# Optimization experiments

Measured on AMD Instinct MI355X. Metric: run time of the kernel, lower is better.

Reference implementation:

```python
import jax, jax.numpy as jnp
import numpy as np

N, F_IN, E = 50000, 256, 1000000
UNITS, HEADS, LAYERS, OUT = 32, 8, 2, 64
D = UNITS * HEADS  # 256


def setup_inputs() -> dict:
    key = jax.random.key(0)
    ks = jax.random.split(key, 12)
    node_states = jax.random.normal(ks[0], (1, N, F_IN), dtype=jnp.float32)
    # edges sorted by source column (required by the tf.repeat/bincount trick)
    src = jnp.sort(jax.random.randint(ks[1], (E,), 0, N, dtype=jnp.int32))
    dst = jax.random.randint(ks[2], (E,), 0, N, dtype=jnp.int32)
    edges = jnp.stack([src, dst], axis=-1)[None]  # [1, E, 2]
    edge_weights = jax.random.uniform(ks[3], (1, E), dtype=jnp.float32)
    pos_cls = jax.random.randint(ks[4], (1, 128), 0, N, dtype=jnp.int32)
    s = 0.05
    Wp = jax.random.normal(ks[5], (F_IN, D), dtype=jnp.float32) * s
    bp = jnp.zeros((D,), dtype=jnp.float32)
    Wk = jax.random.normal(ks[6], (LAYERS, HEADS, D, UNITS), dtype=jnp.float32) * s
    Wa = jax.random.normal(ks[7], (LAYERS, HEADS, 2 * UNITS, 1), dtype=jnp.float32) * s
    Wo = jax.random.normal(ks[8], (D, OUT), dtype=jnp.float32) * s
    bo = jnp.zeros((OUT,), dtype=jnp.float32)
    return {
        "node_states": node_states, "edges": edges, "edge_weights": edge_weights,
        "pos_cls": pos_cls, "Wp": Wp, "bp": bp, "Wk": Wk, "Wa": Wa,
        "Wo": Wo, "bo": bo,
    }


def _gat_head(x, src, dst, ew, W, a, n_nodes):
    xt = x @ W  # [N, U]
    # edge features: concat(src_feat, dst_feat) scaled by edge weight
    ef = jnp.concatenate([xt[src], xt[dst]], axis=-1) * ew[:, None]  # [E, 2U]
    s = jax.nn.leaky_relu((ef @ a)[:, 0], negative_slope=0.2)        # [E]
    s = jnp.exp(jnp.clip(s, -2.0, 2.0))
    ssum = jax.ops.segment_sum(s, src, num_segments=n_nodes)          # [N]
    norm = s / ssum[src]
    return jax.ops.segment_sum(xt[dst] * norm[:, None], src, num_segments=n_nodes)


def reference(node_states, edges, edge_weights, pos_cls, Wp, bp, Wk, Wa, Wo, bo):
    x0 = node_states[0]        # [N, F_in]
    e = edges[0]               # [E, 2]
    ew = edge_weights[0]       # [E]
    src, dst = e[:, 0], e[:, 1]
    n_nodes = x0.shape[0]
    x = jax.nn.relu(x0 @ Wp + bp)  # [N, D]
    n_layers, n_heads = Wk.shape[0], Wk.shape[1]
    for l in range(n_layers):
        heads = [_gat_head(x, src, dst, ew, Wk[l, h], Wa[l, h], n_nodes)
                 for h in range(n_heads)]
        mh = jax.nn.relu(jnp.concatenate(heads, axis=-1))  # [N, D]
        x = mh + x  # residual
    out = x @ Wo + bo
    return out[None]  # [1, N, OUT]
```

## Files before the change

kernel.cpp:

```cpp
#include <hip/hip_runtime.h>
#include <hip/hip_bf16.h>
#include <math.h>

#define N_NODES 50000
#define F_DIM 256
#define NE 1000000
#define N_HEADS 8
#define M_PAD 50048

typedef __attribute__((ext_vector_type(8))) short short8;
typedef __attribute__((ext_vector_type(4))) float floatx4;
typedef __attribute__((ext_vector_type(2))) float floatx2;

__device__ __forceinline__ void load16_lds(const void* g, void* l) {
    __builtin_amdgcn_global_load_lds(
        (const __attribute__((address_space(1))) unsigned int*)(unsigned long long)g,
        (__attribute__((address_space(3))) unsigned int*)(unsigned int)(unsigned long long)l,
        16, 0, 0);
}

__device__ __forceinline__ unsigned int pack2bf(float a, float b) {
    __hip_bfloat16 t0 = __float2bfloat16(a), t1 = __float2bfloat16(b);
    unsigned short u0, u1;
    __builtin_memcpy(&u0, &t0, 2);
    __builtin_memcpy(&u1, &t1, 2);
    return (unsigned int)u0 | ((unsigned int)u1 << 16);
}

__device__ __forceinline__ float bf_lo(unsigned int u) {
    return __uint_as_float(u << 16);
}
__device__ __forceinline__ float bf_hi(unsigned int u) {
    return __uint_as_float(u & 0xffff0000u);
}

__device__ __forceinline__ unsigned int pack4fp8(float x, float y, float z,
                                                 float w) {
    int v = __builtin_amdgcn_cvt_pk_fp8_f32(x, y, 0, false);
    v = __builtin_amdgcn_cvt_pk_fp8_f32(z, w, v, true);
    return (unsigned int)v;
}

__global__ __launch_bounds__(256) void prep_kernel(
    const float* __restrict__ node_states, const int* __restrict__ edges,
    const float* __restrict__ ew, const float* __restrict__ Wp,
    const float* __restrict__ Wk, const float* __restrict__ Wo,
    __hip_bfloat16* __restrict__ xt16, int2* __restrict__ edata,
    __hip_bfloat16* __restrict__ wpT, __hip_bfloat16* __restrict__ wkT,
    __hip_bfloat16* __restrict__ woT, int* __restrict__ row_start) {
    const int b = blockIdx.x;
    const int tid = threadIdx.x;
    if (b < 12500) {
        const size_t i = ((size_t)b * 256 + tid) * 4;
        const float4 v = *(const float4*)(node_states + i);
        uint2 pk;
        pk.x = pack2bf(v.x, v.y);
        pk.y = pack2bf(v.z, v.w);
        *(uint2*)((unsigned short*)xt16 + i) = pk;
    } else if (b < 16407) {
        const int e = (b - 12500) * 256 + tid;
        if (e < NE) {
            int2 d;
            d.x = edges[2 * e + 1];
            d.y = __float_as_int(ew[e]);
            edata[e] = d;
        }
    } else if (b < 17239) {
        const int wb = b - 16407;
        if (wb < 256) {
            int idx = wb * 256 + tid;
            int n = idx >> 8, k = idx & 255;
            wpT[idx] = __float2bfloat16(Wp[k * 256 + n]);
        } else if (wb < 768) {
            int idx = (wb - 256) * 256 + tid;
            int l = idx >> 16, n = (idx >> 8) & 255, k = idx & 255;
            int h = n >> 5, u = n & 31;
            wkT[idx] = __float2bfloat16(Wk[(((l * 8 + h) * 256) + k) * 32 + u]);
        } else {
            int idx = (wb - 768) * 256 + tid;
            int n = idx >> 8, k = idx & 255;
            woT[idx] = __float2bfloat16(Wo[k * 64 + n]);
        }
    } else {
        const int i = (b - 17239) * 256 + tid;
        if (i > N_NODES) return;
        if (i == N_NODES) { row_start[N_NODES] = NE; return; }
        int lo = 0, hi = NE;
        while (lo < hi) {
            int mid = (lo + hi) >> 1;
            if (edges[2 * mid] < i) lo = mid + 1; else hi = mid;
        }
        row_start[i] = lo;
    }
}

template <bool BIAS_RELU, bool FP8OUT, bool ALPHA>
__global__ __launch_bounds__(256) void gemm_mfma(
    const __hip_bfloat16* __restrict__ A16, const __hip_bfloat16* __restrict__ BT,
    const float* __restrict__ bias, void* __restrict__ Y,
    const float* __restrict__ Wa_l, float* __restrict__ a_srcO,
    float* __restrict__ a_dstO) {
    __shared__ __align__(16) short lA[128 * 32];
    __shared__ __align__(16) short lB[128 * 32];
    const int tid = threadIdx.x;
    const int row0 = blockIdx.x * 128;
    const int n0 = blockIdx.y * 128;
    const int w = tid >> 6, l = tid & 63;
    const int wr = w >> 1, wc = w & 1;

    const __hip_bfloat16* gA = A16 + (size_t)(row0 + (tid >> 2)) * 256 + (tid & 3) * 8;
    const __hip_bfloat16* gB = BT + (size_t)(n0 + (tid >> 2)) * 256 + (tid & 3) * 8;
    short* dA = lA + tid * 8;
    short* dB = lB + tid * 8;

    floatx4 acc[4][4] = {};

    const short* pa = lA + (wr * 64 + (l & 15)) * 32 + (l >> 4) * 8;
    const short* pb = lB + (wc * 64 + (l & 15)) * 32 + (l >> 4) * 8;

    for (int kk = 0; kk < 8; ++kk) {
        const int ko = kk * 32;
        load16_lds(gA + ko, dA);
        load16_lds(gA + 64 * 256 + ko, dA + 256 * 8);
        load16_lds(gB + ko, dB);
        load16_lds(gB + 64 * 256 + ko, dB + 256 * 8);
        __syncthreads();
        short8 af[4], bf[4];
#pragma unroll
        for (int t = 0; t < 4; ++t) {
            af[t] = *(const short8*)(pa + t * 16 * 32);
            bf[t] = *(const short8*)(pb + t * 16 * 32);
        }
#pragma unroll
        for (int mt = 0; mt < 4; ++mt)
#pragma unroll
            for (int nt = 0; nt < 4; ++nt)
                acc[mt][nt] = __builtin_amdgcn_mfma_f32_16x16x32_bf16(
                    bf[nt], af[mt], acc[mt][nt], 0, 0, 0);
        __syncthreads();
    }

    const int m_base = row0 + wr * 64 + (l & 15);
    const int n_base = n0 + wc * 64 + ((l >> 4) << 2);
#pragma unroll
    for (int mt = 0; mt < 4; ++mt) {
        const int m = m_base + mt * 16;
        if (m >= N_NODES) continue;
#pragma unroll
        for (int nt = 0; nt < 4; ++nt) {
            const int n = n_base + nt * 16;
            floatx4 v = acc[mt][nt];
            if (BIAS_RELU) {
                const float4 bb = *(const float4*)(bias + n);
                v.x = fmaxf(v.x + bb.x, 0.f);
                v.y = fmaxf(v.y + bb.y, 0.f);
                v.z = fmaxf(v.z + bb.z, 0.f);
                v.w = fmaxf(v.w + bb.w, 0.f);
            }
            if constexpr (FP8OUT) {
                *((unsigned int*)Y + ((((size_t)m << 8) + n) >> 2)) =
                    pack4fp8(v.x, v.y, v.z, v.w);
            } else {
                uint2 pk;
                pk.x = pack2bf(v.x, v.y);
                pk.y = pack2bf(v.z, v.w);
                *(uint2*)((unsigned short*)Y + ((size_t)m << 8) + n) = pk;
            }
        }
    }

    if constexpr (ALPHA) {
        const int lg = l >> 4;
        float4 wS[2][2], wD[2][2];
#pragma unroll
        for (int hl = 0; hl < 2; ++hl) {
            const int h = (n0 >> 5) + wc * 2 + hl;
#pragma unroll
            for (int p = 0; p < 2; ++p) {
                wS[hl][p] = *(const float4*)(Wa_l + h * 64 + p * 16 + lg * 4);
                wD[hl][p] =
                    *(const float4*)(Wa_l + h * 64 + 32 + p * 16 + lg * 4);
            }
        }
        float aS[4][2], aD[4][2];
#pragma unroll
        for (int mt = 0; mt < 4; ++mt)
#pragma unroll
            for (int hl = 0; hl < 2; ++hl) {
                float s = 0.f, d = 0.f;
#pragma unroll
                for (int p = 0; p < 2; ++p) {
                    const floatx4 v = acc[mt][2 * hl + p];
                    const float4 ws = wS[hl][p], wd = wD[hl][p];
                    s += v.x * ws.x + v.y * ws.y + v.z * ws.z + v.w * ws.w;
                    d += v.x * wd.x + v.y * wd.y + v.z * wd.z + v.w * wd.w;
                }
                s += __shfl_xor(s, 16);
                s += __shfl_xor(s, 32);
                d += __shfl_xor(d, 16);
                d += __shfl_xor(d, 32);
                aS[mt][hl] = s;
                aD[mt][hl] = d;
            }
        if (lg == 0) {
#pragma unroll
            for (int mt = 0; mt < 4; ++mt) {
                const int m = m_base + mt * 16;
#pragma unroll
                for (int hl = 0; hl < 2; ++hl) {
                    const int h = (n0 >> 5) + wc * 2 + hl;
                    a_srcO[(size_t)m * 8 + h] = aS[mt][hl];
                    a_dstO[(size_t)m * 8 + h] = aD[mt][hl];
                }
            }
        }
    }
}

__global__ __launch_bounds__(256) void gemm_mfma_out(
    const __hip_bfloat16* __restrict__ A16, const __hip_bfloat16* __restrict__ BT,
    const float* __restrict__ bias, float* __restrict__ out) {
    __shared__ __align__(16) short lA[128 * 32];
    __shared__ __align__(16) short lB[64 * 32];
    const int tid = threadIdx.x;
    const int row0 = blockIdx.x * 128;
    const int w = tid >> 6, l = tid & 63;

    const __hip_bfloat16* gA = A16 + (size_t)(row0 + (tid >> 2)) * 256 + (tid & 3) * 8;
    const __hip_bfloat16* gB = BT + (size_t)(tid >> 2) * 256 + (tid & 3) * 8;
    short* dA = lA + tid * 8;
    short* dB = lB + tid * 8;

    floatx4 acc[2][4] = {};

    const short* pa = lA + (w * 32 + (l & 15)) * 32 + (l >> 4) * 8;
    const short* pb = lB + (l & 15) * 32 + (l >> 4) * 8;

    for (int kk = 0; kk < 8; ++kk) {
        const int ko = kk * 32;
        load16_lds(gA + ko, dA);
        load16_lds(gA + 64 * 256 + ko, dA + 256 * 8);
        load16_lds(gB + ko, dB);
        __syncthreads();
        short8 af[2], bf[4];
#pragma unroll
        for (int t = 0; t < 2; ++t) af[t] = *(const short8*)(pa + t * 16 * 32);
#pragma unroll
        for (int t = 0; t < 4; ++t) bf[t] = *(const short8*)(pb + t * 16 * 32);
#pragma unroll
        for (int mt = 0; mt < 2; ++mt)
#pragma unroll
            for (int nt = 0; nt < 4; ++nt)
                acc[mt][nt] = __builtin_amdgcn_mfma_f32_16x16x32_bf16(
                    bf[nt], af[mt], acc[mt][nt], 0, 0, 0);
        __syncthreads();
    }

    const int m_base = row0 + w * 32 + (l & 15);
    const int n_base = (l >> 4) << 2;
#pragma unroll
    for (int mt = 0; mt < 2; ++mt) {
        const int m = m_base + mt * 16;
        if (m >= N_NODES) continue;
#pragma unroll
        for (int nt = 0; nt < 4; ++nt) {
            const int n = n_base + nt * 16;
            const float4 bb = *(const float4*)(bias + n);
            floatx4 v = acc[mt][nt];
            float4 o = {v.x + bb.x, v.y + bb.y, v.z + bb.z, v.w + bb.w};
            *(float4*)(&out[(size_t)m * 64 + n]) = o;
        }
    }
}

__device__ __forceinline__ float edge_score(float asrc, float ad, float w) {
    float sp = (asrc + ad) * w;
    sp = (sp >= 0.f) ? sp : 0.2f * sp;
    sp = fminf(fmaxf(sp, -2.f), 2.f);
    return __expf(sp);
}

#define ACC8(u, s)                                               \
    {                                                            \
        const floatx2 f01 = __builtin_amdgcn_cvt_pk_f32_fp8(u, false); \
        const floatx2 f23 = __builtin_amdgcn_cvt_pk_f32_fp8(u, true);  \
        a0 = fmaf(f01.x, s, a0);                                 \
        a1 = fmaf(f01.y, s, a1);                                 \
        a2 = fmaf(f23.x, s, a2);                                 \
        a3 = fmaf(f23.y, s, a3);                                 \
    }

__global__ __launch_bounds__(256) void edge_kernel(
    const unsigned long long* __restrict__ edata,
    const int* __restrict__ row_start, const unsigned int* __restrict__ xt8,
    const float* __restrict__ a_src, const float* __restrict__ a_dst,
    __hip_bfloat16* __restrict__ xb16) {
    const int tid = threadIdx.x;
    const int node =
        __builtin_amdgcn_readfirstlane(blockIdx.x * 4 + (tid >> 6));
    const int l = tid & 63;
    const int h = l >> 3;
    const float asrc = a_src[node * N_HEADS + h];
    const int e0 = row_start[node], e1 = row_start[node + 1];

    unsigned long long* xrow =
        (unsigned long long*)((unsigned short*)xb16 + (size_t)node * 256 +
                              l * 4);
    const unsigned long long xin = __builtin_nontemporal_load(xrow);

    float a0 = 0.f, a1 = 0.f, a2 = 0.f, a3 = 0.f, ssum = 0.f;
    int e = e0;
    for (; e + 4 <= e1; e += 4) {
        const unsigned long long ed0 = __builtin_nontemporal_load(edata + e);
        const unsigned long long ed1 = __builtin_nontemporal_load(edata + e + 1);
        const unsigned long long ed2 = __builtin_nontemporal_load(edata + e + 2);
        const unsigned long long ed3 = __builtin_nontemporal_load(edata + e + 3);
        const int d0 = (int)(unsigned int)ed0;
        const int d1 = (int)(unsigned int)ed1;
        const int d2 = (int)(unsigned int)ed2;
        const int d3 = (int)(unsigned int)ed3;
        const float w0 = __uint_as_float((unsigned int)(ed0 >> 32));
        const float w1 = __uint_as_float((unsigned int)(ed1 >> 32));
        const float w2 = __uint_as_float((unsigned int)(ed2 >> 32));
        const float w3 = __uint_as_float((unsigned int)(ed3 >> 32));
        const float s0 = edge_score(asrc, a_dst[d0 * N_HEADS + h], w0);
        const float s1 = edge_score(asrc, a_dst[d1 * N_HEADS + h], w1);
        const float s2 = edge_score(asrc, a_dst[d2 * N_HEADS + h], w2);
        const float s3 = edge_score(asrc, a_dst[d3 * N_HEADS + h], w3);
        const unsigned int u0 = xt8[(size_t)d0 * 64 + l];
        const unsigned int u1 = xt8[(size_t)d1 * 64 + l];
        const unsigned int u2 = xt8[(size_t)d2 * 64 + l];
        const unsigned int u3 = xt8[(size_t)d3 * 64 + l];
        ACC8(u0, s0);
        ACC8(u1, s1);
        ACC8(u2, s2);
        ACC8(u3, s3);
        ssum += (s0 + s1) + (s2 + s3);
    }
    for (; e < e1; ++e) {
        const unsigned long long ed = __builtin_nontemporal_load(edata + e);
        const int d = (int)(unsigned int)ed;
        const float w = __uint_as_float((unsigned int)(ed >> 32));
        const float s = edge_score(asrc, a_dst[d * N_HEADS + h], w);
        const unsigned int u = xt8[(size_t)d * 64 + l];
        ACC8(u, s);
        ssum += s;
    }
    const float inv = (e1 > e0) ? 1.f / ssum : 0.f;
    const unsigned int xlo = (unsigned int)xin;
    const unsigned int xhi = (unsigned int)(xin >> 32);
    const float c0 = bf_lo(xlo) + fmaxf(a0 * inv, 0.f);
    const float c1 = bf_hi(xlo) + fmaxf(a1 * inv, 0.f);
    const float c2 = bf_lo(xhi) + fmaxf(a2 * inv, 0.f);
    const float c3 = bf_hi(xhi) + fmaxf(a3 * inv, 0.f);
    const unsigned long long pk =
        (unsigned long long)pack2bf(c0, c1) |
        ((unsigned long long)pack2bf(c2, c3) << 32);
    __builtin_nontemporal_store(pk, xrow);
}

extern "C" void kernel_launch(void* const* d_in, const int* in_sizes, int n_in,
                              void* d_out, int out_size, void* d_ws,
                              size_t ws_size, hipStream_t stream) {
    const float* node_states = (const float*)d_in[0];
    const int* edges = (const int*)d_in[1];
    const float* ew = (const float*)d_in[2];
    const float* Wp = (const float*)d_in[4];
    const float* bp = (const float*)d_in[5];
    const float* Wk = (const float*)d_in[6];
    const float* Wa = (const float*)d_in[7];
    const float* Wo = (const float*)d_in[8];
    const float* bo = (const float*)d_in[9];
    float* out = (float*)d_out;

    char* ws = (char*)d_ws;
    __hip_bfloat16* xb16 = (__hip_bfloat16*)ws; ws += (size_t)M_PAD * 256 * 2;
    __hip_bfloat16* xt16 = (__hip_bfloat16*)ws; ws += (size_t)M_PAD * 256 * 2;
    unsigned int* xt8 = (unsigned int*)ws;      ws += (size_t)M_PAD * 256;
    int2* edata = (int2*)ws;                    ws += (size_t)NE * 8;
    float* a_src = (float*)ws;                  ws += (size_t)M_PAD * N_HEADS * 4;
    float* a_dst = (float*)ws;                  ws += (size_t)M_PAD * N_HEADS * 4;
    __hip_bfloat16* wpT = (__hip_bfloat16*)ws;  ws += 65536 * 2;
    __hip_bfloat16* wkT = (__hip_bfloat16*)ws;  ws += 131072 * 2;
    __hip_bfloat16* woT = (__hip_bfloat16*)ws;  ws += 16384 * 2;
    int* row_st = (int*)ws;

    prep_kernel<<<17435, 256, 0, stream>>>(node_states, edges, ew, Wp, Wk, Wo,
                                           xt16, edata, wpT, wkT, woT, row_st);

    gemm_mfma<true, false, false><<<dim3((N_NODES + 127) / 128, 2), 256, 0,
                                    stream>>>(xt16, wpT, bp, xb16, nullptr,
                                              nullptr, nullptr);

    gemm_mfma<false, true, true><<<dim3((N_NODES + 127) / 128, 2), 256, 0,
                                   stream>>>(xb16, wkT, nullptr, xt8, Wa,
                                             a_src, a_dst);
    edge_kernel<<<N_NODES / 4, 256, 0, stream>>>(
        (const unsigned long long*)edata, row_st, xt8, a_src, a_dst, xb16);

    gemm_mfma<false, true, true><<<dim3((N_NODES + 127) / 128, 2), 256, 0,
                                   stream>>>(xb16, wkT + 65536, nullptr, xt8,
                                             Wa + 512, a_src, a_dst);
    edge_kernel<<<N_NODES / 4, 256, 0, stream>>>(
        (const unsigned long long*)edata, row_st, xt8, a_src, a_dst, xb16);

    gemm_mfma_out<<<(N_NODES + 127) / 128, 256, 0, stream>>>(xb16, woT, bo, out);
}
```

Before: 298.1 us.

## Compute edge scores cooperatively across lanes and broadcast via bpermute in edge kernel

Each wavefront previously had every lane compute the score of every edge for its own head, which is 8x redundant work per head group. Now the 64 lanes are split into 8 edge slots by 8 heads, so each lane computes one (edge, head) score per batch of 8 edges. Scores are broadcast with ds_bpermute and destination ids with readlane, and the softmax denominator is reduced with xor shuffles. This cuts the redundant a_dst gathers and exp work, at the cost of cross-lane permutes and readlanes on every edge.

Result: no change. 303.7 us (+1.9%).

```diff
diff --git a/kernel.cpp b/kernel.cpp
--- a/kernel.cpp
+++ b/kernel.cpp
@@ -299,53 +299,64 @@
     const int node =
         __builtin_amdgcn_readfirstlane(blockIdx.x * 4 + (tid >> 6));
     const int l = tid & 63;
-    const int h = l >> 3;
-    const float asrc = a_src[node * N_HEADS + h];
-    const int e0 = row_start[node], e1 = row_start[node + 1];
+    const int hf = l >> 3;
+    const int hs = l & 7;
+    const int slot = l >> 3;
+    const int e0 = __builtin_amdgcn_readfirstlane(row_start[node]);
+    const int e1 = __builtin_amdgcn_readfirstlane(row_start[node + 1]);
+    const float asrc = a_src[(size_t)node * 8 + hs];
+    const int baddr = hf << 2;
 
     unsigned long long* xrow =
         (unsigned long long*)((unsigned short*)xb16 + (size_t)node * 256 +
                               l * 4);
     const unsigned long long xin = __builtin_nontemporal_load(xrow);
 
-    float a0 = 0.f, a1 = 0.f, a2 = 0.f, a3 = 0.f, ssum = 0.f;
-    int e = e0;
-    for (; e + 4 <= e1; e += 4) {
-        const unsigned long long ed0 = __builtin_nontemporal_load(edata + e);
-        const unsigned long long ed1 = __builtin_nontemporal_load(edata + e + 1);
-        const unsigned long long ed2 = __builtin_nontemporal_load(edata + e + 2);
-        const unsigned long long ed3 = __builtin_nontemporal_load(edata + e + 3);
-        const int d0 = (int)(unsigned int)ed0;
-        const int d1 = (int)(unsigned int)ed1;
-        const int d2 = (int)(unsigned int)ed2;
-        const int d3 = (int)(unsigned int)ed3;
-        const float w0 = __uint_as_float((unsigned int)(ed0 >> 32));
-        const float w1 = __uint_as_float((unsigned int)(ed1 >> 32));
-        const float w2 = __uint_as_float((unsigned int)(ed2 >> 32));
-        const float w3 = __uint_as_float((unsigned int)(ed3 >> 32));
-        const float s0 = edge_score(asrc, a_dst[d0 * N_HEADS + h], w0);
-        const float s1 = edge_score(asrc, a_dst[d1 * N_HEADS + h], w1);
-        const float s2 = edge_score(asrc, a_dst[d2 * N_HEADS + h], w2);
-        const float s3 = edge_score(asrc, a_dst[d3 * N_HEADS + h], w3);
-        const unsigned int u0 = xt8[(size_t)d0 * 64 + l];
-        const unsigned int u1 = xt8[(size_t)d1 * 64 + l];
-        const unsigned int u2 = xt8[(size_t)d2 * 64 + l];
-        const unsigned int u3 = xt8[(size_t)d3 * 64 + l];
-        ACC8(u0, s0);
-        ACC8(u1, s1);
-        ACC8(u2, s2);
-        ACC8(u3, s3);
-        ssum += (s0 + s1) + (s2 + s3);
-    }
-    for (; e < e1; ++e) {
-        const unsigned long long ed = __builtin_nontemporal_load(edata + e);
-        const int d = (int)(unsigned int)ed;
+    float a0 = 0.f, a1 = 0.f, a2 = 0.f, a3 = 0.f, ssp = 0.f;
+    int eb = e0;
+    for (; eb + 8 <= e1; eb += 8) {
+        const unsigned long long ed =
+            __builtin_nontemporal_load(edata + eb + slot);
+        const int dd = (int)(unsigned int)ed;
         const float w = __uint_as_float((unsigned int)(ed >> 32));
-        const float s = edge_score(asrc, a_dst[d * N_HEADS + h], w);
-        const unsigned int u = xt8[(size_t)d * 64 + l];
-        ACC8(u, s);
-        ssum += s;
-    }
+        const float s = edge_score(asrc, a_dst[(size_t)dd * 8 + hs], w);
+        ssp += s;
+        const int sbits = (int)__float_as_uint(s);
+#pragma unroll
+        for (int j = 0; j < 8; ++j) {
+            const float sj = __uint_as_float(
+                (unsigned int)__builtin_amdgcn_ds_bpermute(baddr + (j << 5),
+                                                           sbits));
+            const int dj = __builtin_amdgcn_readlane(dd, j * 8);
+            const unsigned int u = xt8[(size_t)dj * 64 + l];
+            ACC8(u, sj);
+        }
+    }
+    if (eb < e1) {
+        const int ecl = min(eb + slot, e1 - 1);
+        const unsigned long long ed = __builtin_nontemporal_load(edata + ecl);
+        const int dd = (int)(unsigned int)ed;
+        const float w = __uint_as_float((unsigned int)(ed >> 32));
+        float s = edge_score(asrc, a_dst[(size_t)dd * 8 + hs], w);
+        s = (eb + slot < e1) ? s : 0.f;
+        ssp += s;
+        const int sbits = (int)__float_as_uint(s);
+        const int jmax = e1 - eb;
+        for (int j = 0; j < jmax; ++j) {
+            const float sj = __uint_as_float(
+                (unsigned int)__builtin_amdgcn_ds_bpermute(baddr + (j << 5),
+                                                           sbits));
+            const int dj = __builtin_amdgcn_readlane(dd, j * 8);
+            const unsigned int u = xt8[(size_t)dj * 64 + l];
+            ACC8(u, sj);
+        }
+    }
+    ssp += __shfl_xor(ssp, 8);
+    ssp += __shfl_xor(ssp, 16);
+    ssp += __shfl_xor(ssp, 32);
+    const float ssum = __uint_as_float((unsigned int)__builtin_amdgcn_ds_bpermute(
+        baddr, (int)__float_as_uint(ssp)));
+
     const float inv = (e1 > e0) ? 1.f / ssum : 0.f;
     const unsigned int xlo = (unsigned int)xin;
     const unsigned int xhi = (unsigned int)(xin >> 32);
```
